# Kernel optimization log

Measured on AMD Instinct MI355X. Metric: run time of the kernel, lower is better.

## Reference

```python
import math
import jax, jax.numpy as jnp
import numpy as np

# ---- SLAYER neuron / simulation constants (from config) ----
THETA = 10.0      # spike threshold
TAU_SR = 10.0     # PSP (SRM) kernel time constant
TAU_REF = 1.0     # refractory kernel time constant
TS = 1.0          # simulation time step
T_SAMPLE = 500    # number of time bins
B, N_IN, N_HID, N_OUT = 64, 1024, 1024, 10


def _alpha_kernel(tau, mult, eps=0.01):
    """slayer _calculateAlphaKernel: mult * t/tau * exp(1 - t/tau), truncated."""
    vals = []
    t = 0.0
    while t < T_SAMPLE:
        v = mult * t / tau * math.exp(1.0 - t / tau)
        if abs(v) < eps and t > tau:
            break
        vals.append(v)
        t += TS
    return np.asarray(vals, np.float32)

SRM_KERNEL = jnp.asarray(_alpha_kernel(TAU_SR, 1.0))            # [K]
REF_KERNEL = jnp.asarray(_alpha_kernel(TAU_REF, -2.0 * THETA))  # [Kr], REF_KERNEL[0] == 0


def dense(x, W):
    # per-timestep fully-connected layer (slayer.dense == 1x1x1 conv3d, no bias)
    # x: [B, Nin, T], W: [Nout, Nin] -> [B, Nout, T]
    return jnp.einsum('oi,bit->bot', W, x)


def psp(x):
    # causal temporal convolution with the SRM kernel: out[t] = Ts * sum_k srm[k] * x[t-k]
    Bx, N, T = x.shape
    K = SRM_KERNEL.shape[0]
    k = SRM_KERNEL[::-1].reshape(1, 1, K).astype(x.dtype)  # flip -> true convolution
    y = jax.lax.conv_general_dilated(
        x.reshape(Bx * N, 1, T), k, (1,), [(K - 1, 0)],
        dimension_numbers=('NCH', 'OIH', 'NCH'))
    return y.reshape(Bx, N, T) * TS


def spike_impl(u_in):
    # sequential LIF thresholding with refractory feedback (slayer spike kernel)
    # u_in: [B, N, T] membrane drive; returns (spikes, membrane) both [B, N, T]
    Kr = REF_KERNEL.shape[0]
    # buf[j] is the refractory contribution arriving at step t+j; new spike at t
    # contributes REF_KERNEL[j] at t+j (REF_KERNEL[0]==0), i.e. shifted kernel into buf.
    refk = jnp.concatenate([REF_KERNEL[1:], jnp.zeros((1,), u_in.dtype)]).astype(u_in.dtype)
    buf0 = jnp.zeros(u_in.shape[:-1] + (Kr,), u_in.dtype)

    def step(buf, u_t):
        u = u_t + buf[..., 0]                              # membrane at time t
        s = (u >= THETA).astype(u_in.dtype) / TS           # spike (amplitude 1/Ts)
        buf = jnp.concatenate([buf[..., 1:], jnp.zeros_like(buf[..., :1])], axis=-1)
        buf = buf + s[..., None] * refk
        return buf, (s, u)

    _, (s, u) = jax.lax.scan(step, buf0, jnp.moveaxis(u_in, -1, 0))
    return jnp.moveaxis(s, 0, -1), jnp.moveaxis(u, 0, -1)


def setup_inputs() -> dict:
    key = jax.random.key(0)
    k1, k2, k3 = jax.random.split(key, 3)
    spike_input = (jax.random.uniform(k1, (B, N_IN, T_SAMPLE)) < 0.05).astype(jnp.float32)
    W1 = jax.random.normal(k2, (N_HID, N_IN), jnp.float32) * 0.3
    W2 = jax.random.normal(k3, (N_OUT, N_HID), jnp.float32) * 0.3
    return {"spike_input": spike_input, "W1": W1, "W2": W2}


def reference(spike_input, W1, W2):
    s1, _ = spike_impl(psp(dense(spike_input, W1)))
    s2, _ = spike_impl(psp(dense(s1, W2)))
    return s2
```

## Files before the change

### kernel.cpp

```cpp
#include <hip/hip_runtime.h>
#include <stdint.h>
#include <math.h>

#define T_SIM 500
#define NB    64
#define NIN   1024
#define NHID  1024
#define NOUT  10
#define KSRM  77
#define CHUNK 32
#define TT    32
#define RING  140

__device__ __forceinline__ double srm_tap(int k) {
  double u = (double)k / 10.0;
  double v = u * exp(1.0 - u);
  return (double)(float)v;
}
__device__ __forceinline__ double ref_tap(int j) {
  double v = (-20.0 * (double)j) * exp(1.0 - (double)j);
  return (double)(float)v;
}

__global__ __launch_bounds__(64)
void k_pack(const float* __restrict__ x, unsigned long long* __restrict__ bits) {
  const int b = blockIdx.x, ig = blockIdx.y, tc = blockIdx.z;
  const int lane = threadIdx.x;
  const float* xr = x + ((size_t)b * NIN + ig * 64 + lane) * T_SIM;
  const int t0 = tc * 100;
  for (int t = t0; t < t0 + 100; t += 4) {
    const float4 v = *(const float4*)(xr + t);
    unsigned long long m0 = __ballot(v.x > 0.5f);
    unsigned long long m1 = __ballot(v.y > 0.5f);
    unsigned long long m2 = __ballot(v.z > 0.5f);
    unsigned long long m3 = __ballot(v.w > 0.5f);
    if (lane == 0) {
      unsigned long long* w = bits + (size_t)(b * T_SIM + t) * 16 + ig;
      w[0] = m0; w[16] = m1; w[32] = m2; w[48] = m3;
    }
  }
}

__global__ __launch_bounds__(256)
void k_transpose(const float* __restrict__ W1, float* __restrict__ W1T) {
  __shared__ float tile[64][65];
  const int bo = blockIdx.x * 64, bi = blockIdx.y * 64;
  for (int k = threadIdx.x; k < 4096; k += 256) {
    int r = k >> 6, c = k & 63;
    tile[r][c] = W1[(size_t)(bo + r) * NIN + bi + c];
  }
  __syncthreads();
  for (int k = threadIdx.x; k < 4096; k += 256) {
    int r = k >> 6, c = k & 63;
    W1T[(size_t)(bi + r) * NHID + bo + c] = tile[c][r];
  }
}

__global__ __launch_bounds__(256)
void k_dense1(const uint32_t* __restrict__ bits, const float* __restrict__ W1T,
              double* __restrict__ a1c, int col_base) {
  __shared__ int list[NIN];
  __shared__ int nact_s;
  const int col_loc = blockIdx.x;
  const int tid = threadIdx.x;
  if (tid < 32) {
    uint32_t w = bits[(size_t)(col_base + col_loc) * 32 + tid];
    int c = __popc(w);
    int p = c;
#pragma unroll
    for (int d = 1; d < 32; d <<= 1) {
      int q = __shfl_up(p, d);
      if (tid >= d) p += q;
    }
    int excl = p - c;
    while (w) {
      const int j = __ffs(w) - 1;
      w &= w - 1;
      list[excl++] = tid * 32 + j;
    }
    if (tid == 31) nact_s = excl;
  }
  __syncthreads();
  const int n = nact_s;
  const int o = tid * 4;
  double a0x=0,a0y=0,a0z=0,a0w=0, a1x=0,a1y=0,a1z=0,a1w=0;
  double a2x=0,a2y=0,a2z=0,a2w=0, a3x=0,a3y=0,a3z=0,a3w=0;
  int g = 0;
  for (; g + 4 <= n; g += 4) {
    const int i0 = list[g], i1 = list[g+1], i2 = list[g+2], i3 = list[g+3];
    const float4 w0 = *(const float4*)(W1T + (size_t)i0 * NHID + o);
    const float4 w1 = *(const float4*)(W1T + (size_t)i1 * NHID + o);
    const float4 w2 = *(const float4*)(W1T + (size_t)i2 * NHID + o);
    const float4 w3 = *(const float4*)(W1T + (size_t)i3 * NHID + o);
    a0x += (double)w0.x; a0y += (double)w0.y; a0z += (double)w0.z; a0w += (double)w0.w;
    a1x += (double)w1.x; a1y += (double)w1.y; a1z += (double)w1.z; a1w += (double)w1.w;
    a2x += (double)w2.x; a2y += (double)w2.y; a2z += (double)w2.z; a2w += (double)w2.w;
    a3x += (double)w3.x; a3y += (double)w3.y; a3z += (double)w3.z; a3w += (double)w3.w;
  }
  if (g + 0 < n) {
    const float4 wv = *(const float4*)(W1T + (size_t)list[g+0] * NHID + o);
    a0x += (double)wv.x; a0y += (double)wv.y; a0z += (double)wv.z; a0w += (double)wv.w;
  }
  if (g + 1 < n) {
    const float4 wv = *(const float4*)(W1T + (size_t)list[g+1] * NHID + o);
    a1x += (double)wv.x; a1y += (double)wv.y; a1z += (double)wv.z; a1w += (double)wv.w;
  }
  if (g + 2 < n) {
    const float4 wv = *(const float4*)(W1T + (size_t)list[g+2] * NHID + o);
    a2x += (double)wv.x; a2y += (double)wv.y; a2z += (double)wv.z; a2w += (double)wv.w;
  }
  double4 r;
  r.x = (a0x + a1x) + (a2x + a3x);
  r.y = (a0y + a1y) + (a2y + a3y);
  r.z = (a0z + a1z) + (a2z + a3z);
  r.w = (a0w + a1w) + (a2w + a3w);
  *(double4*)(a1c + (size_t)col_loc * NHID + o) = r;
}

__global__ __launch_bounds__(256)
void k_ps1(const double* __restrict__ a1c, uint32_t* __restrict__ s1w,
           int b_base) {
  __shared__ double S[RING * 32];
  __shared__ double Y[TT * 32];
  __shared__ double srm[KSRM];
  const int ng = blockIdx.x, b_loc = blockIdx.y;
  const int tid = threadIdx.x;
  if (tid < KSRM) srm[tid] = srm_tap(tid);

  double refk[11];
#pragma unroll
  for (int j = 1; j <= 10; ++j) refk[j] = ref_tap(j);
  uint32_t smask = 0;

  const double* __restrict__ abase = a1c + (size_t)b_loc * T_SIM * NHID + ng * 32;
  uint32_t* __restrict__ sbase =
      s1w + (size_t)(b_base + b_loc) * T_SIM * 32 + ng;

  double pf[4];
  {
#pragma unroll
    for (int j = 0; j < 4; ++j) {
      const int id = tid + j * 256;
      const int r = id >> 5, n = id & 31;
      pf[j] = abase[(size_t)r * NHID + n];
    }
    for (int i = tid; i < RING * 32; i += 256) S[i] = 0.0;
    __syncthreads();
#pragma unroll
    for (int j = 0; j < 4; ++j) {
      const int id = tid + j * 256;
      const int r = id >> 5, n = id & 31;
      S[((r) % RING) * 32 + n] = pf[j];
    }
    __syncthreads();
  }

  for (int t0 = 0; t0 < T_SIM; t0 += TT) {
    const int tv = (T_SIM - t0 < TT) ? (T_SIM - t0) : TT;
    const int t0n = t0 + TT;
    const int tvn = (t0n >= T_SIM) ? 0 : ((T_SIM - t0n < TT) ? (T_SIM - t0n) : TT);
#pragma unroll
    for (int j = 0; j < 4; ++j) {
      const int id = tid + j * 256;
      if (id < tvn * 32) {
        const int r = id >> 5, n = id & 31;
        pf[j] = abase[(size_t)(t0n + r) * NHID + n];
      }
    }
    {
      const int n = tid & 31, tq = tid >> 5;
      const int tbase = t0 + tq * 4 - 76;
      int m0 = tbase % RING; if (m0 < 0) m0 += RING;
      int len1 = RING - m0; if (len1 > 80) len1 = 80;
      double tap0 = 0.0, tap1 = 0.0, tap2 = 0.0, tap3 = 0.0;
      double c0 = 0.0, c1 = 0.0, c2 = 0.0, c3 = 0.0;
      int s = 0;
#pragma unroll 4
      for (; s < len1; ++s) {
        const double v = S[(m0 + s) * 32 + n];
        tap3 = tap2; tap2 = tap1; tap1 = tap0;
        tap0 = (s <= 76) ? srm[76 - s] : 0.0;
        c0 += tap0 * v; c1 += tap1 * v; c2 += tap2 * v; c3 += tap3 * v;
      }
#pragma unroll 4
      for (; s < 80; ++s) {
        const double v = S[(s - len1) * 32 + n];
        tap3 = tap2; tap2 = tap1; tap1 = tap0;
        tap0 = (s <= 76) ? srm[76 - s] : 0.0;
        c0 += tap0 * v; c1 += tap1 * v; c2 += tap2 * v; c3 += tap3 * v;
      }
      const int tl = tq * 4;
      if (tl + 0 < tv) Y[(tl + 0) * 32 + n] = c0;
      if (tl + 1 < tv) Y[(tl + 1) * 32 + n] = c1;
      if (tl + 2 < tv) Y[(tl + 2) * 32 + n] = c2;
      if (tl + 3 < tv) Y[(tl + 3) * 32 + n] = c3;
    }
    __syncthreads();
    if (tid < 32) {
      for (int g = 0; g < tv; ++g) {
        double u = Y[g * 32 + tid];
#pragma unroll
        for (int j = 10; j >= 1; --j)
          u += refk[j] * (double)((smask >> (j - 1)) & 1u);
        const bool sp = (u >= 10.0);
        smask = (smask << 1) | (sp ? 1u : 0u);
        const unsigned long long bm = __ballot(sp);
        if (tid == 0) sbase[(size_t)(t0 + g) * 32] = (uint32_t)bm;
      }
    }
#pragma unroll
    for (int j = 0; j < 4; ++j) {
      const int id = tid + j * 256;
      if (id < tvn * 32) {
        const int r = id >> 5, n = id & 31;
        S[((t0n + r) % RING) * 32 + n] = pf[j];
      }
    }
    __syncthreads();
  }
}

__global__ __launch_bounds__(256)
void k_dense2(const uint32_t* __restrict__ s1w,
              const float* __restrict__ W2, double* __restrict__ a2) {
  __shared__ float w2t[NHID * NOUT];
  for (int k = threadIdx.x; k < NHID * NOUT; k += 256) {
    const int o = k >> 10, i = k & 1023;
    w2t[i * NOUT + o] = W2[k];
  }
  __syncthreads();
  const int col = blockIdx.x * 256 + threadIdx.x;
  double acc[NOUT];
#pragma unroll
  for (int o = 0; o < NOUT; ++o) acc[o] = 0.0;
  const uint32_t* w = s1w + (size_t)col * 32;
  for (int wi = 0; wi < 32; ++wi) {
    uint32_t m = w[wi];
    const int ibase = wi * 32;
    while (m) {
      const int j = __ffs(m) - 1;
      m &= m - 1;
      const float* row = &w2t[(ibase + j) * NOUT];
#pragma unroll
      for (int o = 0; o < NOUT; ++o) acc[o] += (double)row[o];
    }
  }
  double* outp = a2 + (size_t)col * NOUT;
#pragma unroll
  for (int o = 0; o < NOUT; ++o) outp[o] = acc[o];
}

__global__ __launch_bounds__(256)
void k_l2(const double* __restrict__ a2, float* __restrict__ out) {
  __shared__ double S[T_SIM * NOUT];
  __shared__ double Y[T_SIM * NOUT];
  __shared__ double srm[KSRM];
  const int b = blockIdx.x, tid = threadIdx.x;
  if (tid < KSRM) srm[tid] = srm_tap(tid);
  for (int i = tid; i < T_SIM * NOUT; i += 256)
    S[i] = a2[(size_t)b * T_SIM * NOUT + i];
  __syncthreads();
  for (int i = tid; i < T_SIM * NOUT; i += 256) {
    const int t = i / 10, o = i - t * 10;
    const int kmax = (t < KSRM - 1) ? t : (KSRM - 1);
    double acc = 0.0;
    for (int k = 0; k <= kmax; ++k)
      acc += srm[k] * S[(t - k) * 10 + o];
    Y[i] = acc;
  }
  __syncthreads();
  if (tid < NOUT) {
    double refk[11];
#pragma unroll
    for (int j = 1; j <= 10; ++j) refk[j] = ref_tap(j);
    uint32_t smask = 0;
    float* op = out + ((size_t)b * NOUT + tid) * T_SIM;
    for (int t = 0; t < T_SIM; ++t) {
      double u = Y[t * 10 + tid];
#pragma unroll
      for (int j = 10; j >= 1; --j)
        u += refk[j] * (double)((smask >> (j - 1)) & 1u);
      const bool sp = (u >= 10.0);
      smask = (smask << 1) | (sp ? 1u : 0u);
      op[t] = sp ? 1.0f : 0.0f;
    }
  }
}

extern "C" void kernel_launch(void* const* d_in, const int* in_sizes, int n_in,
                              void* d_out, int out_size, void* d_ws, size_t ws_size,
                              hipStream_t stream) {
  const float* x  = (const float*)d_in[0];
  const float* W1 = (const float*)d_in[1];
  const float* W2 = (const float*)d_in[2];
  float* out = (float*)d_out;

  char* ws = (char*)d_ws;
  unsigned long long* bits1 = (unsigned long long*)(ws);
  float*  W1T = (float*) (ws + 4096000);
  double* a1c = (double*)(ws + 8290304);
  uint32_t* s1w = (uint32_t*)(ws + 139362304);
  double* a2  = (double*)(ws + 143458304);

  hipLaunchKernelGGL(k_pack, dim3(NB, 16, 5), dim3(64), 0, stream, x, bits1);
  hipLaunchKernelGGL(k_transpose, dim3(16, 16), dim3(256), 0, stream, W1, W1T);

  for (int bc = 0; bc < NB; bc += CHUNK) {
    hipLaunchKernelGGL(k_dense1, dim3(CHUNK * T_SIM), dim3(256), 0, stream,
                       (const uint32_t*)bits1, W1T, a1c, bc * T_SIM);
    hipLaunchKernelGGL(k_ps1, dim3(32, CHUNK), dim3(256), 0, stream,
                       a1c, s1w, bc);
  }

  hipLaunchKernelGGL(k_dense2, dim3(125), dim3(256), 0, stream, s1w, W2, a2);
  hipLaunchKernelGGL(k_l2, dim3(NB), dim3(256), 0, stream, a2, out);
}
```

Baseline: 1.093 ms.

## Warp-specialize PSP/spike kernel and software-pipeline gathered W1 loads

Splits the PSP+spike block into one spike-threshold wavefront that processes the previous tile while three wavefronts compute the SRM convolution for the current tile into a double-buffered Y. The sequential thresholding now overlaps the convolution instead of serializing with it. Tiles grow to 36 steps, the ring buffer to 148 slots, and the convolution register-blocks 6 outputs per thread with a rotating tap window. The dense1 gather loop also prefetches the next four W1 rows before accumulating the current ones. This adds register pressure and leaves fewer threads for the convolution.

```diff
diff --git a/kernel.cpp b/kernel.cpp
--- a/kernel.cpp
+++ b/kernel.cpp
@@ -9,8 +9,9 @@
 #define NOUT  10
 #define KSRM  77
 #define CHUNK 32
-#define TT    32
-#define RING  140
+#define TT2   36
+#define NT    14
+#define RING2 148
 
 __device__ __forceinline__ double srm_tap(int k) {
   double u = (double)k / 10.0;
@@ -85,17 +86,28 @@
   const int o = tid * 4;
   double a0x=0,a0y=0,a0z=0,a0w=0, a1x=0,a1y=0,a1z=0,a1w=0;
   double a2x=0,a2y=0,a2z=0,a2w=0, a3x=0,a3y=0,a3z=0,a3w=0;
+  float4 L0, L1, L2, L3;
   int g = 0;
+  if (g + 4 <= n) {
+    L0 = *(const float4*)(W1T + (size_t)list[0] * NHID + o);
+    L1 = *(const float4*)(W1T + (size_t)list[1] * NHID + o);
+    L2 = *(const float4*)(W1T + (size_t)list[2] * NHID + o);
+    L3 = *(const float4*)(W1T + (size_t)list[3] * NHID + o);
+  }
   for (; g + 4 <= n; g += 4) {
-    const int i0 = list[g], i1 = list[g+1], i2 = list[g+2], i3 = list[g+3];
-    const float4 w0 = *(const float4*)(W1T + (size_t)i0 * NHID + o);
-    const float4 w1 = *(const float4*)(W1T + (size_t)i1 * NHID + o);
-    const float4 w2 = *(const float4*)(W1T + (size_t)i2 * NHID + o);
-    const float4 w3 = *(const float4*)(W1T + (size_t)i3 * NHID + o);
-    a0x += (double)w0.x; a0y += (double)w0.y; a0z += (double)w0.z; a0w += (double)w0.w;
-    a1x += (double)w1.x; a1y += (double)w1.y; a1z += (double)w1.z; a1w += (double)w1.w;
-    a2x += (double)w2.x; a2y += (double)w2.y; a2z += (double)w2.z; a2w += (double)w2.w;
-    a3x += (double)w3.x; a3y += (double)w3.y; a3z += (double)w3.z; a3w += (double)w3.w;
+    float4 N0, N1, N2, N3;
+    const bool more = (g + 8 <= n);
+    if (more) {
+      N0 = *(const float4*)(W1T + (size_t)list[g+4] * NHID + o);
+      N1 = *(const float4*)(W1T + (size_t)list[g+5] * NHID + o);
+      N2 = *(const float4*)(W1T + (size_t)list[g+6] * NHID + o);
+      N3 = *(const float4*)(W1T + (size_t)list[g+7] * NHID + o);
+    }
+    a0x += (double)L0.x; a0y += (double)L0.y; a0z += (double)L0.z; a0w += (double)L0.w;
+    a1x += (double)L1.x; a1y += (double)L1.y; a1z += (double)L1.z; a1w += (double)L1.w;
+    a2x += (double)L2.x; a2y += (double)L2.y; a2z += (double)L2.z; a2w += (double)L2.w;
+    a3x += (double)L3.x; a3y += (double)L3.y; a3z += (double)L3.z; a3w += (double)L3.w;
+    if (more) { L0 = N0; L1 = N1; L2 = N2; L3 = N3; }
   }
   if (g + 0 < n) {
     const float4 wv = *(const float4*)(W1T + (size_t)list[g+0] * NHID + o);
@@ -120,103 +132,124 @@
 __global__ __launch_bounds__(256)
 void k_ps1(const double* __restrict__ a1c, uint32_t* __restrict__ s1w,
            int b_base) {
-  __shared__ double S[RING * 32];
-  __shared__ double Y[TT * 32];
-  __shared__ double srm[KSRM];
+  __shared__ double S[RING2 * 32];
+  __shared__ double Y[2][TT2 * 32];
+  __shared__ double TB[87];
   const int ng = blockIdx.x, b_loc = blockIdx.y;
   const int tid = threadIdx.x;
-  if (tid < KSRM) srm[tid] = srm_tap(tid);
+
+  const double* __restrict__ abase = a1c + (size_t)b_loc * T_SIM * NHID + ng * 32;
+  uint32_t* __restrict__ sbase = s1w + (size_t)(b_base + b_loc) * T_SIM * 32 + ng;
+
+  if (tid < 87) {
+    double v = 0.0;
+    if (tid >= 5 && tid <= 81) v = srm_tap(tid - 5);
+    TB[tid] = v;
+  }
+  for (int i = tid; i < RING2 * 32; i += 256) S[i] = 0.0;
+  __syncthreads();
+  for (int id = tid; id < TT2 * 32; id += 256) {
+    const int r = id >> 5, nn = id & 31;
+    S[r * 32 + nn] = abase[(size_t)r * NHID + nn];
+  }
+  __syncthreads();
 
   double refk[11];
 #pragma unroll
   for (int j = 1; j <= 10; ++j) refk[j] = ref_tap(j);
   uint32_t smask = 0;
 
-  const double* __restrict__ abase = a1c + (size_t)b_loc * T_SIM * NHID + ng * 32;
-  uint32_t* __restrict__ sbase =
-      s1w + (size_t)(b_base + b_loc) * T_SIM * 32 + ng;
-
-  double pf[4];
-  {
-#pragma unroll
-    for (int j = 0; j < 4; ++j) {
-      const int id = tid + j * 256;
-      const int r = id >> 5, n = id & 31;
-      pf[j] = abase[(size_t)r * NHID + n];
-    }
-    for (int i = tid; i < RING * 32; i += 256) S[i] = 0.0;
+  for (int k = 0; k < NT; ++k) {
+    const int t0 = k * TT2;
+    const int tv = (T_SIM - t0 < TT2) ? (T_SIM - t0) : TT2;
+    const int t0n = t0 + TT2;
+    const int tvn = (t0n >= T_SIM) ? 0 : ((T_SIM - t0n < TT2) ? (T_SIM - t0n) : TT2);
+    if (tid >= 64) {
+      const int f = tid - 64;
+      double pf[6];
+#pragma unroll
+      for (int j = 0; j < 6; ++j) {
+        const int id = f + j * 192;
+        if (id < tvn * 32) {
+          const int r = id >> 5, nn = id & 31;
+          pf[j] = abase[(size_t)(t0n + r) * NHID + nn];
+        }
+      }
+      const int n = f & 31, tq = f >> 5;
+      const int tb = t0 + tq * 6;
+      int m0 = (tb - 76) % RING2; if (m0 < 0) m0 += RING2;
+      double acc[6] = {0, 0, 0, 0, 0, 0};
+      double tr[6];
+#pragma unroll
+      for (int e = 81; e <= 86; ++e) tr[e % 6] = TB[e];
+      int idx = m0;
+      for (int sb = 0; sb < 78; sb += 6) {
+#pragma unroll
+        for (int r = 0; r < 6; ++r) {
+          const int s = sb + r;
+          const double v = S[idx * 32 + n];
+          idx = (idx + 1 == RING2) ? 0 : idx + 1;
+#pragma unroll
+          for (int u = 0; u < 6; ++u)
+            acc[u] += tr[(9 - r + u) % 6] * v;
+          tr[(8 - r) % 6] = TB[80 - s];
+        }
+      }
+#pragma unroll
+      for (int r = 0; r < 4; ++r) {
+        const int s = 78 + r;
+        const double v = S[idx * 32 + n];
+        idx = (idx + 1 == RING2) ? 0 : idx + 1;
+#pragma unroll
+        for (int u = 0; u < 6; ++u)
+          acc[u] += tr[(9 - r + u) % 6] * v;
+        if (r < 3) tr[(8 - r) % 6] = TB[80 - s];
+      }
+      const int tl0 = tq * 6;
+      double* Yk = Y[k & 1];
+#pragma unroll
+      for (int u = 0; u < 6; ++u)
+        if (tl0 + u < tv) Yk[(tl0 + u) * 32 + n] = acc[u];
+#pragma unroll
+      for (int j = 0; j < 6; ++j) {
+        const int id = f + j * 192;
+        if (id < tvn * 32) {
+          const int r = id >> 5, nn = id & 31;
+          S[((t0n + r) % RING2) * 32 + nn] = pf[j];
+        }
+      }
+    } else if (k > 0) {
+      if (tid < 32) {
+        const int t0p = (k - 1) * TT2;
+        const double* Yp = Y[(k - 1) & 1];
+        for (int g = 0; g < TT2; ++g) {
+          double u = Yp[g * 32 + tid];
+#pragma unroll
+          for (int j = 10; j >= 1; --j)
+            u += refk[j] * (double)((smask >> (j - 1)) & 1u);
+          const bool sp = (u >= 10.0);
+          smask = (smask << 1) | (sp ? 1u : 0u);
+          const unsigned long long bm = __ballot(sp);
+          if (tid == 0) sbase[(size_t)(t0p + g) * 32] = (uint32_t)bm;
+        }
+      }
+    }
     __syncthreads();
-#pragma unroll
-    for (int j = 0; j < 4; ++j) {
-      const int id = tid + j * 256;
-      const int r = id >> 5, n = id & 31;
-      S[((r) % RING) * 32 + n] = pf[j];
-    }
-    __syncthreads();
-  }
-
-  for (int t0 = 0; t0 < T_SIM; t0 += TT) {
-    const int tv = (T_SIM - t0 < TT) ? (T_SIM - t0) : TT;
-    const int t0n = t0 + TT;
-    const int tvn = (t0n >= T_SIM) ? 0 : ((T_SIM - t0n < TT) ? (T_SIM - t0n) : TT);
-#pragma unroll
-    for (int j = 0; j < 4; ++j) {
-      const int id = tid + j * 256;
-      if (id < tvn * 32) {
-        const int r = id >> 5, n = id & 31;
-        pf[j] = abase[(size_t)(t0n + r) * NHID + n];
-      }
-    }
-    {
-      const int n = tid & 31, tq = tid >> 5;
-      const int tbase = t0 + tq * 4 - 76;
-      int m0 = tbase % RING; if (m0 < 0) m0 += RING;
-      int len1 = RING - m0; if (len1 > 80) len1 = 80;
-      double tap0 = 0.0, tap1 = 0.0, tap2 = 0.0, tap3 = 0.0;
-      double c0 = 0.0, c1 = 0.0, c2 = 0.0, c3 = 0.0;
-      int s = 0;
-#pragma unroll 4
-      for (; s < len1; ++s) {
-        const double v = S[(m0 + s) * 32 + n];
-        tap3 = tap2; tap2 = tap1; tap1 = tap0;
-        tap0 = (s <= 76) ? srm[76 - s] : 0.0;
-        c0 += tap0 * v; c1 += tap1 * v; c2 += tap2 * v; c3 += tap3 * v;
-      }
-#pragma unroll 4
-      for (; s < 80; ++s) {
-        const double v = S[(s - len1) * 32 + n];
-        tap3 = tap2; tap2 = tap1; tap1 = tap0;
-        tap0 = (s <= 76) ? srm[76 - s] : 0.0;
-        c0 += tap0 * v; c1 += tap1 * v; c2 += tap2 * v; c3 += tap3 * v;
-      }
-      const int tl = tq * 4;
-      if (tl + 0 < tv) Y[(tl + 0) * 32 + n] = c0;
-      if (tl + 1 < tv) Y[(tl + 1) * 32 + n] = c1;
-      if (tl + 2 < tv) Y[(tl + 2) * 32 + n] = c2;
-      if (tl + 3 < tv) Y[(tl + 3) * 32 + n] = c3;
-    }
-    __syncthreads();
-    if (tid < 32) {
-      for (int g = 0; g < tv; ++g) {
-        double u = Y[g * 32 + tid];
-#pragma unroll
-        for (int j = 10; j >= 1; --j)
-          u += refk[j] * (double)((smask >> (j - 1)) & 1u);
-        const bool sp = (u >= 10.0);
-        smask = (smask << 1) | (sp ? 1u : 0u);
-        const unsigned long long bm = __ballot(sp);
-        if (tid == 0) sbase[(size_t)(t0 + g) * 32] = (uint32_t)bm;
-      }
-    }
-#pragma unroll
-    for (int j = 0; j < 4; ++j) {
-      const int id = tid + j * 256;
-      if (id < tvn * 32) {
-        const int r = id >> 5, n = id & 31;
-        S[((t0n + r) % RING) * 32 + n] = pf[j];
-      }
-    }
-    __syncthreads();
+  }
+  if (tid < 32) {
+    const int t0p = (NT - 1) * TT2;
+    const int tvp = T_SIM - t0p;
+    const double* Yp = Y[(NT - 1) & 1];
+    for (int g = 0; g < tvp; ++g) {
+      double u = Yp[g * 32 + tid];
+#pragma unroll
+      for (int j = 10; j >= 1; --j)
+        u += refk[j] * (double)((smask >> (j - 1)) & 1u);
+      const bool sp = (u >= 10.0);
+      smask = (smask << 1) | (sp ? 1u : 0u);
+      const unsigned long long bm = __ballot(sp);
+      if (tid == 0) sbase[(size_t)(t0p + g) * 32] = (uint32_t)bm;
+    }
   }
 }
 
```

Measured after the change: 1.171 ms. 1.07x slower.
